# Kernel tuning notes

Measured on AMD Instinct MI355X. Metric: run time of the kernel, lower is better.

The kernel has to match this reference:

```python
import jax, jax.numpy as jnp
import numpy as np

SR = 48000
MAX_DUR = 5.0
N_AUDIO = 480000  # 10 s @ 48 kHz
K_IR = int(SR * MAX_DUR)  # 240000 taps


def setup_inputs() -> dict:
    key = jax.random.key(0)
    k1, k2 = jax.random.split(key)
    audio = jax.random.normal(k1, (N_AUDIO,), dtype=jnp.float32)
    impulse_response = jax.random.normal(k2, (K_IR,), dtype=jnp.float32)
    return {"audio": audio, "impulse_response": impulse_response}


def reference(audio, impulse_response):
    # torch: pad audio with (K-1) zeros, then conv1d (= cross-correlation, no flip)
    K = impulse_response.shape[0]
    a_pad = jnp.concatenate([audio, jnp.zeros((K - 1,), dtype=audio.dtype)])
    # out[t] = sum_k a_pad[t+k] * ir[k], valid correlation -> length N
    out = jnp.correlate(a_pad, impulse_response, mode="valid")
    # trailing peak normalization
    return out / jnp.max(jnp.abs(out))
```

## Files before the change

kernel.cpp:

```cpp
#include <hip/hip_runtime.h>

typedef unsigned int u32;


constexpr int N_AUDIO = 480000;
constexpr int K_IR    = 240000;
constexpr int M_FFT   = 1048576;

constexpr size_t OFF_C0   = 0;
constexpr size_t OFF_C1   = (size_t)M_FFT * 8;
constexpr size_t OFF_SLOT = OFF_C1 + (size_t)M_FFT * 8;

#define SW(i) ((i) + ((i) >> 4))
constexpr int LSZ = 1088;

struct F2 { float x, y; };
constexpr double D_PI = 3.14159265358979323846264338327950288;
constexpr double tay_sin(double x) {
    double t = x, s = x, x2 = x * x;
    for (int k = 1; k <= 11; ++k) { t *= -x2 / (double)((2 * k) * (2 * k + 1)); s += t; }
    return s;
}
constexpr double tay_cos(double x) {
    double t = 1.0, s = 1.0, x2 = x * x;
    for (int k = 1; k <= 11; ++k) { t *= -x2 / (double)((2 * k - 1) * (2 * k)); s += t; }
    return s;
}
struct Tab { F2 v[1024]; };
constexpr Tab make_t1() {
    Tab tb{};
    for (int j = 0; j < 1024; ++j) {
        int jj = (j < 512) ? j : j - 1024;
        double a = -2.0 * D_PI * (double)jj / 1024.0;
        tb.v[j] = F2{(float)tay_cos(a), (float)tay_sin(a)};
    }
    return tb;
}
constexpr Tab make_t2() {
    Tab tb{};
    for (int j = 0; j < 1024; ++j) {
        double a = -2.0 * D_PI * (double)j / 1048576.0;
        tb.v[j] = F2{(float)tay_cos(a), (float)tay_sin(a)};
    }
    return tb;
}
__device__ constexpr Tab ROM_T1 = make_t1();
__device__ constexpr Tab ROM_T2 = make_t2();

__device__ __forceinline__ float2 ldrom(const Tab& tb, int i) {
    F2 f = tb.v[i];
    return make_float2(f.x, f.y);
}
__device__ __forceinline__ float2 cmul(float2 a, float2 b) {
    return make_float2(a.x * b.x - a.y * b.y, a.x * b.y + a.y * b.x);
}

template<int NB>
__device__ __forceinline__ void fft1024_r4(float2 (*A0)[LSZ], float2 (*B0)[LSZ],
                                           const float2* lt1, int t) {
    float2 (*A)[LSZ] = A0;
    float2 (*B)[LSZ] = B0;
    #pragma unroll
    for (int s = 0; s < 5; ++s) {
        const int L  = 1 << (2 * s);
        const int k  = t & (L - 1);
        const int p0 = 4 * t - 3 * k;
        const float2 w  = lt1[k << (9 - 2 * s)];
        const float2 w2 = lt1[k << (8 - 2 * s)];
        #pragma unroll
        for (int j = 0; j < NB; ++j) {
            float2 x0 = A[j][SW(t)];
            float2 x2 = A[j][SW(t + 256)];
            float2 x1 = A[j][SW(t + 512)];
            float2 x3 = A[j][SW(t + 768)];
            float2 wx1 = cmul(w, x1), wx3 = cmul(w, x3);
            float2 u0 = make_float2(x0.x + wx1.x, x0.y + wx1.y);
            float2 u1 = make_float2(x0.x - wx1.x, x0.y - wx1.y);
            float2 u2 = make_float2(x2.x + wx3.x, x2.y + wx3.y);
            float2 u3 = make_float2(x2.x - wx3.x, x2.y - wx3.y);
            float2 a2 = cmul(w2, u2);
            float2 a3 = cmul(w2, u3);
            B[j][SW(p0)]         = make_float2(u0.x + a2.x, u0.y + a2.y);
            B[j][SW(p0 + L)]     = make_float2(u1.x + a3.y, u1.y - a3.x);
            B[j][SW(p0 + 2*L)]   = make_float2(u0.x - a2.x, u0.y - a2.y);
            B[j][SW(p0 + 3*L)]   = make_float2(u1.x - a3.y, u1.y + a3.x);
        }
        __syncthreads();
        float2 (*tmp)[LSZ] = A; A = B; B = tmp;
    }
}

__global__ __launch_bounds__(256) void fft1_p1(const float* __restrict__ a,
                                               const float* __restrict__ b,
                                               float2* __restrict__ outb,
                                               u32* __restrict__ slot) {
    __shared__ float2 rows[2][LSZ], scr[2][LSZ], lt1[1024], lt2[1024];
    const int t  = threadIdx.x;
    const int r0 = blockIdx.x * 2;
    if (blockIdx.x == 0 && t == 0) *slot = 0u;
    #pragma unroll
    for (int q = 0; q < 4; ++q) {
        int i = t + 256 * q;
        lt1[i] = ldrom(ROM_T1, i);
        lt2[i] = ldrom(ROM_T2, i);
    }
    #pragma unroll
    for (int q = 0; q < 4; ++q) {
        int c = t + 256 * q;
        int base = c * 1024 + r0;
        float2 av = make_float2(0.f, 0.f), bv = make_float2(0.f, 0.f);
        if (c < 468 || (c == 468 && r0 < 768)) av = *(const float2*)(a + base);
        if (c < 234 || (c == 234 && r0 < 384)) bv = *(const float2*)(b + base);
        rows[0][SW(c)] = make_float2(av.x, bv.x);
        rows[1][SW(c)] = make_float2(av.y, bv.y);
    }
    __syncthreads();
    fft1024_r4<2>(rows, scr, lt1, t);
    #pragma unroll
    for (int q = 0; q < 4; ++q) {
        int k1 = t + 256 * q;
        #pragma unroll
        for (int j = 0; j < 2; ++j) {
            int e = (r0 + j) * k1;
            float2 w = cmul(lt1[e >> 10], lt2[e & 1023]);
            outb[(r0 + j) * 1024 + k1] = cmul(w, scr[j][SW(k1)]);
        }
    }
}

__global__ __launch_bounds__(256) void fft1_p2_pw(const float2* __restrict__ in,
                                                  float2* __restrict__ spec) {
    __shared__ float2 cols[2][LSZ], scr[2][LSZ], lt1[1024];
    const int t = threadIdx.x;
    const int bidx = blockIdx.x;
    const int cA = (bidx == 0) ? 0   : bidx;
    const int cB = (bidx == 0) ? 512 : 1024 - bidx;
    #pragma unroll
    for (int q = 0; q < 4; ++q) { int i = t + 256 * q; lt1[i] = ldrom(ROM_T1, i); }
    #pragma unroll
    for (int q = 0; q < 4; ++q) {
        int r = t + 256 * q;
        cols[0][SW(r)] = in[r * 1024 + cA];
        cols[1][SW(r)] = in[r * 1024 + cB];
    }
    __syncthreads();
    fft1024_r4<2>(cols, scr, lt1, t);
    const float invM = 1.0f / 1048576.0f;
    #pragma unroll
    for (int q = 0; q < 4; ++q) {
        int k2 = t + 256 * q;
        #pragma unroll
        for (int j = 0; j < 2; ++j) {
            float2 z1 = scr[j][SW(k2)];
            float2 z2;
            if (bidx == 0) z2 = (j == 0) ? scr[0][SW((1024 - k2) & 1023)]
                                         : scr[1][SW(1023 - k2)];
            else           z2 = scr[j ^ 1][SW(1023 - k2)];
            float2 Af  = make_float2(0.5f * (z1.x + z2.x), 0.5f * (z1.y - z2.y));
            float2 cBf = make_float2(0.5f * (z1.y + z2.y), 0.5f * (z1.x - z2.x));
            float2 S   = cmul(Af, cBf);
            int cc = (j == 0) ? cA : cB;
            spec[cc * 1024 + k2] = make_float2(S.x * invM, -S.y * invM);
        }
    }
}

__global__ __launch_bounds__(256) void fft2_p1(const float2* __restrict__ in,
                                               float2* __restrict__ outb) {
    __shared__ float2 rows[2][LSZ], scr[2][LSZ], lt1[1024], lt2[1024];
    const int t  = threadIdx.x;
    const int r0 = blockIdx.x * 2;
    #pragma unroll
    for (int q = 0; q < 4; ++q) {
        int i = t + 256 * q;
        lt1[i] = ldrom(ROM_T1, i);
        lt2[i] = ldrom(ROM_T2, i);
    }
    const float4* inv4 = (const float4*)(in + (size_t)r0 * 1024);
    #pragma unroll
    for (int q = 0; q < 4; ++q) {
        int i2 = t + 256 * q;
        float4 v = inv4[i2];
        int j = i2 >> 9, c = (i2 & 511) * 2;
        rows[j][SW(c)]     = make_float2(v.x, v.y);
        rows[j][SW(c + 1)] = make_float2(v.z, v.w);
    }
    __syncthreads();
    fft1024_r4<2>(rows, scr, lt1, t);
    #pragma unroll
    for (int q = 0; q < 4; ++q) {
        int k1 = t + 256 * q;
        #pragma unroll
        for (int j = 0; j < 2; ++j) {
            int e = (r0 + j) * k1;
            float2 w = cmul(lt1[e >> 10], lt2[e & 1023]);
            outb[(r0 + j) * 1024 + k1] = cmul(w, scr[j][SW(k1)]);
        }
    }
}

__global__ __launch_bounds__(256) void fft2_p2(const float2* __restrict__ in,
                                               float* __restrict__ rawT,
                                               u32* __restrict__ slot) {
    __shared__ float2 cols[2][LSZ], scr[2][LSZ], lt1[1024];
    __shared__ float wmax[4];
    const int t  = threadIdx.x;
    const int c0 = blockIdx.x * 2;
    #pragma unroll
    for (int q = 0; q < 4; ++q) { int i = t + 256 * q; lt1[i] = ldrom(ROM_T1, i); }
    #pragma unroll
    for (int q = 0; q < 4; ++q) {
        int r = t + 256 * q;
        float4 v = *(const float4*)(in + (size_t)r * 1024 + c0);
        cols[0][SW(r)] = make_float2(v.x, v.y);
        cols[1][SW(r)] = make_float2(v.z, v.w);
    }
    __syncthreads();
    fft1024_r4<2>(cols, scr, lt1, t);
    float m = 0.0f;
    #pragma unroll
    for (int q = 0; q < 4; ++q) {
        int k2 = t + 256 * q;
        #pragma unroll
        for (int j = 0; j < 2; ++j) {
            int ot = c0 + j + (k2 << 10);
            if (ot < N_AUDIO) {
                float v = scr[j][SW(k2)].x;
                rawT[(c0 + j) * 512 + k2] = v;
                m = fmaxf(m, fabsf(v));
            }
        }
    }
    for (int off = 32; off > 0; off >>= 1) m = fmaxf(m, __shfl_down(m, off, 64));
    if ((t & 63) == 0) wmax[t >> 6] = m;
    __syncthreads();
    if (t == 0) {
        float bm = fmaxf(fmaxf(wmax[0], wmax[1]), fmaxf(wmax[2], wmax[3]));
        atomicMax(slot, __float_as_uint(bm));
    }
}

__global__ __launch_bounds__(256) void scale_t(const float* __restrict__ rawT,
                                               const u32* __restrict__ slot,
                                               float* __restrict__ out) {
    __shared__ float tile[64][65];
    const int t  = threadIdx.x;
    const int c0 = (blockIdx.x & 15) * 64;
    const int k0 = (blockIdx.x >> 4) * 64;
    const int cl = t >> 2, ch = (t & 3) * 16;
    #pragma unroll
    for (int i = 0; i < 4; ++i) {
        float4 v = *(const float4*)(rawT + (size_t)(c0 + cl) * 512 + k0 + ch + i * 4);
        tile[cl][ch + i * 4 + 0] = v.x;
        tile[cl][ch + i * 4 + 1] = v.y;
        tile[cl][ch + i * 4 + 2] = v.z;
        tile[cl][ch + i * 4 + 3] = v.w;
    }
    __syncthreads();
    const float inv = 1.0f / __uint_as_float(*slot);
    const int cw = t & 63, w = t >> 6;
    #pragma unroll
    for (int q = 0; q < 16; ++q) {
        int kk = q * 4 + w;
        int o = (k0 + kk) * 1024 + c0 + cw;
        if (o < N_AUDIO) out[o] = tile[cw][kk] * inv;
    }
}

extern "C" void kernel_launch(void* const* d_in, const int* in_sizes, int n_in,
                              void* d_out, int out_size, void* d_ws, size_t ws_size,
                              hipStream_t stream) {
    const float* audio = (const float*)d_in[0];
    const float* ir    = (const float*)d_in[1];
    float* out = (float*)d_out;

    char* ws = (char*)d_ws;
    float2* cb0 = (float2*)(ws + OFF_C0);
    float2* cb1 = (float2*)(ws + OFF_C1);
    u32*    slot = (u32*)(ws + OFF_SLOT);

    fft1_p1<<<512, 256, 0, stream>>>(audio, ir, cb1, slot);
    fft1_p2_pw<<<512, 256, 0, stream>>>(cb1, cb0);
    fft2_p1<<<512, 256, 0, stream>>>(cb0, cb1);
    fft2_p2<<<512, 256, 0, stream>>>(cb1, (float*)cb0, slot);
    scale_t<<<128, 256, 0, stream>>>((const float*)cb0, slot, out);
}
```

Before: 109.4 us.

## Fuse pointwise spectrum product with inverse FFT column pass in one kernel

Merges the forward second-pass FFT, the spectral multiply and the inverse FFT's first pass into a single kernel operating on the same column pair in shared memory. Each block's inverse first pass runs over its two columns and writes twiddled results transposed, which removes one full 8 MB round trip through global memory and one kernel launch. This relies on the four-step decomposition allowing the inverse first pass to act on columns, and kD reads the output accordingly. The cost is a longer kernel with more shared memory use (lt2 is now staged) and potentially lower occupancy, and the scattered output write pattern may coalesce less well.

```diff
diff --git a/kernel.cpp b/kernel.cpp
--- a/kernel.cpp
+++ b/kernel.cpp
@@ -4,7 +4,6 @@
 
 
 constexpr int N_AUDIO = 480000;
-constexpr int K_IR    = 240000;
 constexpr int M_FFT   = 1048576;
 
 constexpr size_t OFF_C0   = 0;
@@ -54,8 +53,15 @@
 __device__ __forceinline__ float2 cmul(float2 a, float2 b) {
     return make_float2(a.x * b.x - a.y * b.y, a.x * b.y + a.y * b.x);
 }
-
-template<int NB>
+__device__ __forceinline__ void stage_tabs(float2* lt1, float2* lt2, int t) {
+    #pragma unroll
+    for (int q = 0; q < 4; ++q) {
+        int i = t + 256 * q;
+        lt1[i] = ldrom(ROM_T1, i);
+        lt2[i] = ldrom(ROM_T2, i);
+    }
+}
+
 __device__ __forceinline__ void fft1024_r4(float2 (*A0)[LSZ], float2 (*B0)[LSZ],
                                            const float2* lt1, int t) {
     float2 (*A)[LSZ] = A0;
@@ -68,7 +74,7 @@
         const float2 w  = lt1[k << (9 - 2 * s)];
         const float2 w2 = lt1[k << (8 - 2 * s)];
         #pragma unroll
-        for (int j = 0; j < NB; ++j) {
+        for (int j = 0; j < 2; ++j) {
             float2 x0 = A[j][SW(t)];
             float2 x2 = A[j][SW(t + 256)];
             float2 x1 = A[j][SW(t + 512)];
@@ -90,20 +96,15 @@
     }
 }
 
-__global__ __launch_bounds__(256) void fft1_p1(const float* __restrict__ a,
-                                               const float* __restrict__ b,
-                                               float2* __restrict__ outb,
-                                               u32* __restrict__ slot) {
-    __shared__ float2 rows[2][LSZ], scr[2][LSZ], lt1[1024], lt2[1024];
+__global__ __launch_bounds__(256) void kA(const float* __restrict__ a,
+                                          const float* __restrict__ b,
+                                          float2* __restrict__ outb,
+                                          u32* __restrict__ slot) {
+    __shared__ float2 buf0[2][LSZ], buf1[2][LSZ], lt1[1024], lt2[1024];
     const int t  = threadIdx.x;
     const int r0 = blockIdx.x * 2;
     if (blockIdx.x == 0 && t == 0) *slot = 0u;
-    #pragma unroll
-    for (int q = 0; q < 4; ++q) {
-        int i = t + 256 * q;
-        lt1[i] = ldrom(ROM_T1, i);
-        lt2[i] = ldrom(ROM_T2, i);
-    }
+    stage_tabs(lt1, lt2, t);
     #pragma unroll
     for (int q = 0; q < 4; ++q) {
         int c = t + 256 * q;
@@ -111,11 +112,11 @@
         float2 av = make_float2(0.f, 0.f), bv = make_float2(0.f, 0.f);
         if (c < 468 || (c == 468 && r0 < 768)) av = *(const float2*)(a + base);
         if (c < 234 || (c == 234 && r0 < 384)) bv = *(const float2*)(b + base);
-        rows[0][SW(c)] = make_float2(av.x, bv.x);
-        rows[1][SW(c)] = make_float2(av.y, bv.y);
-    }
-    __syncthreads();
-    fft1024_r4<2>(rows, scr, lt1, t);
+        buf0[0][SW(c)] = make_float2(av.x, bv.x);
+        buf0[1][SW(c)] = make_float2(av.y, bv.y);
+    }
+    __syncthreads();
+    fft1024_r4(buf0, buf1, lt1, t);
     #pragma unroll
     for (int q = 0; q < 4; ++q) {
         int k1 = t + 256 * q;
@@ -123,86 +124,63 @@
         for (int j = 0; j < 2; ++j) {
             int e = (r0 + j) * k1;
             float2 w = cmul(lt1[e >> 10], lt2[e & 1023]);
-            outb[(r0 + j) * 1024 + k1] = cmul(w, scr[j][SW(k1)]);
-        }
-    }
-}
-
-__global__ __launch_bounds__(256) void fft1_p2_pw(const float2* __restrict__ in,
-                                                  float2* __restrict__ spec) {
-    __shared__ float2 cols[2][LSZ], scr[2][LSZ], lt1[1024];
+            outb[(r0 + j) * 1024 + k1] = cmul(w, buf1[j][SW(k1)]);
+        }
+    }
+}
+
+__global__ __launch_bounds__(256) void kBC(const float2* __restrict__ in,
+                                           float2* __restrict__ outb) {
+    __shared__ float2 buf0[2][LSZ], buf1[2][LSZ], lt1[1024], lt2[1024];
     const int t = threadIdx.x;
     const int bidx = blockIdx.x;
     const int cA = (bidx == 0) ? 0   : bidx;
     const int cB = (bidx == 0) ? 512 : 1024 - bidx;
-    #pragma unroll
-    for (int q = 0; q < 4; ++q) { int i = t + 256 * q; lt1[i] = ldrom(ROM_T1, i); }
+    stage_tabs(lt1, lt2, t);
     #pragma unroll
     for (int q = 0; q < 4; ++q) {
         int r = t + 256 * q;
-        cols[0][SW(r)] = in[r * 1024 + cA];
-        cols[1][SW(r)] = in[r * 1024 + cB];
-    }
-    __syncthreads();
-    fft1024_r4<2>(cols, scr, lt1, t);
+        buf0[0][SW(r)] = in[r * 1024 + cA];
+        buf0[1][SW(r)] = in[r * 1024 + cB];
+    }
+    __syncthreads();
+    fft1024_r4(buf0, buf1, lt1, t);
     const float invM = 1.0f / 1048576.0f;
     #pragma unroll
     for (int q = 0; q < 4; ++q) {
         int k2 = t + 256 * q;
         #pragma unroll
         for (int j = 0; j < 2; ++j) {
-            float2 z1 = scr[j][SW(k2)];
+            float2 z1 = buf1[j][SW(k2)];
             float2 z2;
-            if (bidx == 0) z2 = (j == 0) ? scr[0][SW((1024 - k2) & 1023)]
-                                         : scr[1][SW(1023 - k2)];
-            else           z2 = scr[j ^ 1][SW(1023 - k2)];
+            if (bidx == 0) z2 = (j == 0) ? buf1[0][SW((1024 - k2) & 1023)]
+                                         : buf1[1][SW(1023 - k2)];
+            else           z2 = buf1[j ^ 1][SW(1023 - k2)];
             float2 Af  = make_float2(0.5f * (z1.x + z2.x), 0.5f * (z1.y - z2.y));
             float2 cBf = make_float2(0.5f * (z1.y + z2.y), 0.5f * (z1.x - z2.x));
             float2 S   = cmul(Af, cBf);
+            buf0[j][SW(k2)] = make_float2(S.x * invM, -S.y * invM);
+        }
+    }
+    __syncthreads();
+    fft1024_r4(buf0, buf1, lt1, t);
+    #pragma unroll
+    for (int q = 0; q < 4; ++q) {
+        int k1 = t + 256 * q;
+        #pragma unroll
+        for (int j = 0; j < 2; ++j) {
             int cc = (j == 0) ? cA : cB;
-            spec[cc * 1024 + k2] = make_float2(S.x * invM, -S.y * invM);
-        }
-    }
-}
-
-__global__ __launch_bounds__(256) void fft2_p1(const float2* __restrict__ in,
-                                               float2* __restrict__ outb) {
-    __shared__ float2 rows[2][LSZ], scr[2][LSZ], lt1[1024], lt2[1024];
-    const int t  = threadIdx.x;
-    const int r0 = blockIdx.x * 2;
-    #pragma unroll
-    for (int q = 0; q < 4; ++q) {
-        int i = t + 256 * q;
-        lt1[i] = ldrom(ROM_T1, i);
-        lt2[i] = ldrom(ROM_T2, i);
-    }
-    const float4* inv4 = (const float4*)(in + (size_t)r0 * 1024);
-    #pragma unroll
-    for (int q = 0; q < 4; ++q) {
-        int i2 = t + 256 * q;
-        float4 v = inv4[i2];
-        int j = i2 >> 9, c = (i2 & 511) * 2;
-        rows[j][SW(c)]     = make_float2(v.x, v.y);
-        rows[j][SW(c + 1)] = make_float2(v.z, v.w);
-    }
-    __syncthreads();
-    fft1024_r4<2>(rows, scr, lt1, t);
-    #pragma unroll
-    for (int q = 0; q < 4; ++q) {
-        int k1 = t + 256 * q;
-        #pragma unroll
-        for (int j = 0; j < 2; ++j) {
-            int e = (r0 + j) * k1;
+            int e  = cc * k1;
             float2 w = cmul(lt1[e >> 10], lt2[e & 1023]);
-            outb[(r0 + j) * 1024 + k1] = cmul(w, scr[j][SW(k1)]);
-        }
-    }
-}
-
-__global__ __launch_bounds__(256) void fft2_p2(const float2* __restrict__ in,
-                                               float* __restrict__ rawT,
-                                               u32* __restrict__ slot) {
-    __shared__ float2 cols[2][LSZ], scr[2][LSZ], lt1[1024];
+            outb[cc * 1024 + k1] = cmul(w, buf1[j][SW(k1)]);
+        }
+    }
+}
+
+__global__ __launch_bounds__(256) void kD(const float2* __restrict__ in,
+                                          float* __restrict__ rawT,
+                                          u32* __restrict__ slot) {
+    __shared__ float2 buf0[2][LSZ], buf1[2][LSZ], lt1[1024];
     __shared__ float wmax[4];
     const int t  = threadIdx.x;
     const int c0 = blockIdx.x * 2;
@@ -212,11 +190,11 @@
     for (int q = 0; q < 4; ++q) {
         int r = t + 256 * q;
         float4 v = *(const float4*)(in + (size_t)r * 1024 + c0);
-        cols[0][SW(r)] = make_float2(v.x, v.y);
-        cols[1][SW(r)] = make_float2(v.z, v.w);
-    }
-    __syncthreads();
-    fft1024_r4<2>(cols, scr, lt1, t);
+        buf0[0][SW(r)] = make_float2(v.x, v.y);
+        buf0[1][SW(r)] = make_float2(v.z, v.w);
+    }
+    __syncthreads();
+    fft1024_r4(buf0, buf1, lt1, t);
     float m = 0.0f;
     #pragma unroll
     for (int q = 0; q < 4; ++q) {
@@ -225,7 +203,7 @@
         for (int j = 0; j < 2; ++j) {
             int ot = c0 + j + (k2 << 10);
             if (ot < N_AUDIO) {
-                float v = scr[j][SW(k2)].x;
+                float v = buf1[j][SW(k2)].x;
                 rawT[(c0 + j) * 512 + k2] = v;
                 m = fmaxf(m, fabsf(v));
             }
@@ -240,9 +218,9 @@
     }
 }
 
-__global__ __launch_bounds__(256) void scale_t(const float* __restrict__ rawT,
-                                               const u32* __restrict__ slot,
-                                               float* __restrict__ out) {
+__global__ __launch_bounds__(256) void kE(const float* __restrict__ rawT,
+                                          const u32* __restrict__ slot,
+                                          float* __restrict__ out) {
     __shared__ float tile[64][65];
     const int t  = threadIdx.x;
     const int c0 = (blockIdx.x & 15) * 64;
@@ -279,9 +257,8 @@
     float2* cb1 = (float2*)(ws + OFF_C1);
     u32*    slot = (u32*)(ws + OFF_SLOT);
 
-    fft1_p1<<<512, 256, 0, stream>>>(audio, ir, cb1, slot);
-    fft1_p2_pw<<<512, 256, 0, stream>>>(cb1, cb0);
-    fft2_p1<<<512, 256, 0, stream>>>(cb0, cb1);
-    fft2_p2<<<512, 256, 0, stream>>>(cb1, (float*)cb0, slot);
-    scale_t<<<128, 256, 0, stream>>>((const float*)cb0, slot, out);
-}
+    kA<<<512, 256, 0, stream>>>(audio, ir, cb1, slot);
+    kBC<<<512, 256, 0, stream>>>(cb1, cb0);
+    kD<<<512, 256, 0, stream>>>(cb0, (float*)cb1, slot);
+    kE<<<128, 256, 0, stream>>>((const float*)cb1, slot, out);
+}
```

Result: faster. 104.4 us (-4.5%).
